# Optimization experiments

Measured on AMD Instinct MI355X. Metric: run time of the kernel, lower is better.

The kernel has to match this reference:

```python
import jax, jax.numpy as jnp
import numpy as np

DIM = 1024
HEADS = 16
HEAD_DIM = DIM // HEADS
MLP_HID = 4 * DIM
EPS = 1e-5


def layer_norm(x, g, b):
    mu = jnp.mean(x, axis=-1, keepdims=True)
    var = jnp.mean(jnp.square(x - mu), axis=-1, keepdims=True)
    return (x - mu) * jax.lax.rsqrt(var + EPS) * g + b


def setup_inputs() -> dict:
    key = jax.random.key(0)
    ks = jax.random.split(key, 8)
    s_in = 1.0 / np.sqrt(DIM)
    s_hid = 1.0 / np.sqrt(MLP_HID)
    return {
        "x": jax.random.normal(ks[0], (4, 2048, DIM), dtype=jnp.float32),
        "qkv_w": jax.random.uniform(ks[1], (3 * DIM, DIM), jnp.float32, -s_in, s_in),
        "proj_w": jax.random.uniform(ks[2], (DIM, DIM), jnp.float32, -s_in, s_in),
        "proj_b": jnp.zeros((DIM,), jnp.float32),
        "ln1_g": jnp.ones((DIM,), jnp.float32),
        "ln1_b": jnp.zeros((DIM,), jnp.float32),
        "w1": jax.random.uniform(ks[3], (MLP_HID, DIM), jnp.float32, -s_in, s_in),
        "b1": jnp.zeros((MLP_HID,), jnp.float32),
        "prelu_a": jnp.asarray(0.25, jnp.float32),
        "w2": jax.random.uniform(ks[4], (DIM, MLP_HID), jnp.float32, -s_hid, s_hid),
        "b2": jnp.zeros((DIM,), jnp.float32),
        "ln2_g": jnp.ones((DIM,), jnp.float32),
        "ln2_b": jnp.zeros((DIM,), jnp.float32),
    }


def reference(x, qkv_w, proj_w, proj_b, ln1_g, ln1_b, w1, b1, prelu_a, w2, b2, ln2_g, ln2_b):
    B, N, C = x.shape
    scale = HEAD_DIM ** (-0.5)

    # Multi-head self-attention (full NxN scores, softmax over keys)
    qkv = (x @ qkv_w.T).reshape(B, N, 3, HEADS, HEAD_DIM)
    qkv = jnp.transpose(qkv, (2, 0, 3, 1, 4))  # [3, B, H, N, hd]
    q, k, v = qkv[0] * scale, qkv[1], qkv[2]
    attn = jax.nn.softmax(jnp.einsum("bhnd,bhmd->bhnm", q, k), axis=-1)
    o = jnp.einsum("bhnm,bhmd->bhnd", attn, v)
    o = jnp.transpose(o, (0, 2, 1, 3)).reshape(B, N, C)
    o = o @ proj_w.T + proj_b

    # Post-norm residual 1
    x = layer_norm(x + o, ln1_g, ln1_b)

    # MLP: Linear -> (Dropout=identity in eval) -> PReLU -> Linear
    h = x @ w1.T + b1
    h = jnp.where(h >= 0, h, prelu_a * h)
    h = h @ w2.T + b2

    # Post-norm residual 2
    return layer_norm(x + h, ln2_g, ln2_b)
```

## Files before the change

### kernel.cpp

```cpp
#include <hip/hip_runtime.h>


typedef __attribute__((ext_vector_type(8))) short short8;
typedef __attribute__((ext_vector_type(4))) short short4v;
typedef __attribute__((ext_vector_type(4))) float floatx4;
typedef __attribute__((ext_vector_type(4))) int int4v;

__device__ __forceinline__ float bf2f(unsigned short u) {
    return __uint_as_float(((unsigned int)u) << 16);
}
__device__ __forceinline__ unsigned short f2bf(float f) {
    unsigned int u = __float_as_uint(f);
    u += 0x7FFFu + ((u >> 16) & 1u);
    return (unsigned short)(u >> 16);
}
__device__ __forceinline__ int pack2bf(float a, float b) {
    return (int)f2bf(a) | ((int)f2bf(b) << 16);
}
__device__ __forceinline__ unsigned int cvt_pk_bf16(float lo, float hi) {
    unsigned int r;
    asm("v_cvt_pk_bf16_f32 %0, %1, %2" : "=v"(r) : "v"(lo), "v"(hi));
    return r;
}

#define Q_PRESCALE 0.18033688011112043f

#if __has_builtin(__builtin_amdgcn_exp2f)
__device__ __forceinline__ float fast_exp2(float x) { return __builtin_amdgcn_exp2f(x); }
#else
__device__ __forceinline__ float fast_exp2(float x) { return __expf(x * 0.6931471805599453f); }
#endif

#if __has_builtin(__builtin_amdgcn_permlane32_swap) && __has_builtin(__builtin_amdgcn_permlane16_swap)
#define HAVE_PERMLANE 1
#else
#define HAVE_PERMLANE 0
#endif

__device__ __forceinline__ void async16(const unsigned short* g, unsigned short* l) {
    __builtin_amdgcn_global_load_lds(
        (const __attribute__((address_space(1))) unsigned int*)g,
        (__attribute__((address_space(3))) unsigned int*)l, 16, 0, 0);
}

#define BARRIER() do { __builtin_amdgcn_s_barrier(); asm volatile("" ::: "memory"); } while (0)
#define VMCNT(n)  asm volatile("s_waitcnt vmcnt(" #n ")" ::: "memory")
#define LGKM0()   asm volatile("s_waitcnt lgkmcnt(0)" ::: "memory")

__global__ __launch_bounds__(256)
void cvt_all(const float* __restrict__ x, const float* __restrict__ qkv_w,
             const float* __restrict__ proj_w, const float* __restrict__ w1,
             const float* __restrict__ w2,
             unsigned short* __restrict__ xb, unsigned short* __restrict__ wb) {
    const int b = blockIdx.x;
    const float* src;
    unsigned short* dst;
    size_t doff;
    if (b < 8192) {
        src = x + (size_t)b * 1024; dst = xb; doff = (size_t)b * 1024;
    } else {
        const int wk = b - 8192;
        dst = wb; doff = (size_t)wk * 1024;
        if (wk < 3072)      src = qkv_w  + (size_t)wk * 1024;
        else if (wk < 4096) src = proj_w + (size_t)(wk - 3072) * 1024;
        else if (wk < 8192) src = w1     + (size_t)(wk - 4096) * 1024;
        else                src = w2     + (size_t)(wk - 8192) * 1024;
    }
    const int t4 = threadIdx.x * 4;
    float4 v = *(const float4*)&src[t4];
    short4v o;
    o[0] = (short)f2bf(v.x); o[1] = (short)f2bf(v.y);
    o[2] = (short)f2bf(v.z); o[3] = (short)f2bf(v.w);
    *(short4v*)&dst[doff + t4] = o;
}

__global__ __launch_bounds__(512, 2)
void gemm128(const unsigned short* __restrict__ A,
             const unsigned short* __restrict__ W,
             const float* __restrict__ bias,
             const float* __restrict__ prelu,
             unsigned short* __restrict__ C,
             int N, int K, int qcols, int NNT) {
    __shared__ alignas(16) unsigned short lA[2][128 * 64];
    __shared__ alignas(16) unsigned short lB[2][256 * 64];

    const int nwg = gridDim.x;
    const int orig = blockIdx.x;
    const int q8 = nwg >> 3, r8 = nwg & 7, xx = orig & 7, rest = orig >> 3;
    const int wgid = (xx < r8 ? xx * (q8 + 1) : r8 * (q8 + 1) + (xx - r8) * q8) + rest;
    const int mt = wgid / NNT, nt = wgid % NNT;
    const int m0 = mt * 128, n0 = nt * 256;

    const int tid  = threadIdx.x;
    const int lane = tid & 63;
    const int wave = tid >> 6;
    const int lr = lane & 15, lq = lane >> 4;
    const int wrow = (wave >> 2) * 64;
    const int wcol = (wave & 3) * 32;
    const int srow = lane >> 3;
    const int scol = ((lane & 7) ^ srow) << 3;
    const int kx = lr & 7;

    const int NT = K >> 6;

    floatx4 acc[2][4][2] = {};
    short8 af[4][2], b0[2][2], b1[2][2];

    auto stA = [&](int d, int tt) {
        #pragma unroll
        for (int it = 0; it < 2; ++it) {
            const int rb = (wave * 2 + it) * 8;
            async16(&A[(size_t)(m0 + rb + srow) * K + tt * 64 + scol], &lA[d][rb * 64]);
        }
    };
    auto stB = [&](int d, int tt, int h) {
        #pragma unroll
        for (int it = 0; it < 2; ++it) {
            const int rb = (wave * 2 + it) * 8;
            async16(&W[(size_t)(n0 + h * 128 + rb + srow) * K + tt * 64 + scol],
                    &lB[d][(h * 128 + rb) * 64]);
        }
    };

#define RD_AF(dd)                                                              \
    _Pragma("unroll") for (int i = 0; i < 4; ++i)                              \
    _Pragma("unroll") for (int s = 0; s < 2; ++s)                              \
        af[i][s] = *(const short8*)&lA[dd][(wrow + i * 16 + lr) * 64 +         \
                                           (((s * 4 + lq) ^ kx) << 3)]
#define RD_B0(dd)                                                              \
    _Pragma("unroll") for (int j = 0; j < 2; ++j)                              \
    _Pragma("unroll") for (int s = 0; s < 2; ++s)                              \
        b0[j][s] = *(const short8*)&lB[dd][(wcol + j * 16 + lr) * 64 +         \
                                           (((s * 4 + lq) ^ kx) << 3)]
#define RD_B1(dd)                                                              \
    _Pragma("unroll") for (int j = 0; j < 2; ++j)                              \
    _Pragma("unroll") for (int s = 0; s < 2; ++s)                              \
        b1[j][s] = *(const short8*)&lB[dd][(128 + wcol + j * 16 + lr) * 64 +   \
                                           (((s * 4 + lq) ^ kx) << 3)]
#define MM128(nh, BB)                                                          \
    _Pragma("unroll") for (int s = 0; s < 2; ++s)                              \
    _Pragma("unroll") for (int i = 0; i < 4; ++i)                              \
    _Pragma("unroll") for (int j = 0; j < 2; ++j)                              \
        acc[nh][i][j] = __builtin_amdgcn_mfma_f32_16x16x32_bf16(               \
            af[i][s], BB[j][s], acc[nh][i][j], 0, 0, 0)

    stA(0, 0); stB(0, 0, 0); stB(0, 0, 1);
    stA(1, 1); stB(1, 1, 0);
    VMCNT(4);
    BARRIER();

    auto tile = [&](int t, int d, int e) {
        RD_AF(d);
        RD_B0(d);
        if (t + 1 < NT) stB(e, t + 1, 1);
        BARRIER();
        LGKM0();
        __builtin_amdgcn_s_setprio(1);
        MM128(0, b0);
        __builtin_amdgcn_s_setprio(0);
        BARRIER();

        RD_B1(d);
        if (t + 2 < NT) { stA(d, t + 2); stB(d, t + 2, 0); }
        BARRIER();
        LGKM0();
        __builtin_amdgcn_s_setprio(1);
        MM128(1, b1);
        __builtin_amdgcn_s_setprio(0);
        if (t + 2 < NT)      { VMCNT(4); }
        else if (t + 1 < NT) { VMCNT(0); }
        BARRIER();
    };

    for (int t = 0; t < NT; t += 2) {
        tile(t, 0, 1);
        tile(t + 1, 1, 0);
    }

#undef RD_AF
#undef RD_B0
#undef RD_B1
#undef MM128

    const bool hasb = (bias != nullptr);
    const bool hasp = (prelu != nullptr);
    const float slope = hasp ? prelu[0] : 0.f;
    #pragma unroll
    for (int nh = 0; nh < 2; ++nh)
        #pragma unroll
        for (int j = 0; j < 2; ++j) {
            const int gc = n0 + nh * 128 + wcol + j * 16 + lr;
            const float bv = hasb ? bias[gc] : 0.f;
            const float cs = (gc < qcols) ? Q_PRESCALE : 1.f;
            #pragma unroll
            for (int i = 0; i < 4; ++i) {
                const int gr = m0 + wrow + i * 16 + lq * 4;
                #pragma unroll
                for (int r = 0; r < 4; ++r) {
                    float v = acc[nh][i][j][r] + bv;
                    if (hasp && v < 0.f) v *= slope;
                    C[(size_t)(gr + r) * N + gc] = f2bf(v * cs);
                }
            }
        }
}

__global__ __launch_bounds__(256, 2)
void gemm_sq(const unsigned short* __restrict__ A,
             const unsigned short* __restrict__ W,
             const float* __restrict__ bias,
             const float* __restrict__ prelu,
             unsigned short* __restrict__ C,
             int N, int K, int qcols, int NNT) {
    __shared__ alignas(16) unsigned short lA[2][128 * 64];
    __shared__ alignas(16) unsigned short lB[2][128 * 64];

    const int nwg = gridDim.x;
    const int orig = blockIdx.x;
    const int q8 = nwg >> 3, r8 = nwg & 7, xx = orig & 7, rest = orig >> 3;
    const int wgid = (xx < r8 ? xx * (q8 + 1) : r8 * (q8 + 1) + (xx - r8) * q8) + rest;
    const int mt = wgid / NNT, nt = wgid % NNT;
    const int m0 = mt * 128, n0 = nt * 128;

    const int tid  = threadIdx.x;
    const int lane = tid & 63;
    const int wave = tid >> 6;
    const int lr = lane & 15, lq = lane >> 4;
    const int wrow = (wave >> 1) * 64;
    const int wcol = (wave & 1) * 64;
    const int srow = lane >> 3;
    const int scol = ((lane & 7) ^ srow) << 3;
    const int kx = lr & 7;

    const int NT = K >> 6;

    floatx4 acc[4][4] = {};
    short8 af[4][2], b0[2][2], b1[2][2];

    auto stA = [&](int d, int tt) {
        #pragma unroll
        for (int it = 0; it < 4; ++it) {
            const int rb = it * 32 + wave * 8;
            async16(&A[(size_t)(m0 + rb + srow) * K + tt * 64 + scol], &lA[d][rb * 64]);
        }
    };
    auto stB = [&](int d, int tt) {
        #pragma unroll
        for (int it = 0; it < 4; ++it) {
            const int rb = it * 32 + wave * 8;
            async16(&W[(size_t)(n0 + rb + srow) * K + tt * 64 + scol], &lB[d][rb * 64]);
        }
    };

#define RD_AF(dd)                                                              \
    _Pragma("unroll") for (int i = 0; i < 4; ++i)                              \
    _Pragma("unroll") for (int s = 0; s < 2; ++s)                              \
        af[i][s] = *(const short8*)&lA[dd][(wrow + i * 16 + lr) * 64 +         \
                                           (((s * 4 + lq) ^ kx) << 3)]
#define RD_B0(dd)                                                              \
    _Pragma("unroll") for (int j = 0; j < 2; ++j)                              \
    _Pragma("unroll") for (int s = 0; s < 2; ++s)                              \
        b0[j][s] = *(const short8*)&lB[dd][(wcol + j * 16 + lr) * 64 +         \
                                           (((s * 4 + lq) ^ kx) << 3)]
#define RD_B1(dd)                                                              \
    _Pragma("unroll") for (int j = 0; j < 2; ++j)                              \
    _Pragma("unroll") for (int s = 0; s < 2; ++s)                              \
        b1[j][s] = *(const short8*)&lB[dd][(wcol + 32 + j * 16 + lr) * 64 +    \
                                           (((s * 4 + lq) ^ kx) << 3)]
#define MMSQ(jb, BB)                                                           \
    _Pragma("unroll") for (int s = 0; s < 2; ++s)                              \
    _Pragma("unroll") for (int i = 0; i < 4; ++i)                              \
    _Pragma("unroll") for (int j = 0; j < 2; ++j)                              \
        acc[i][(jb) + j] = __builtin_amdgcn_mfma_f32_16x16x32_bf16(            \
            af[i][s], BB[j][s], acc[i][(jb) + j], 0, 0, 0)

    stA(0, 0); stB(0, 0);
    VMCNT(0);
    BARRIER();

    auto tile = [&](int t, int d, int e) {
        RD_AF(d);
        RD_B0(d);
        if (t + 1 < NT) stA(e, t + 1);
        BARRIER();
        LGKM0();
        __builtin_amdgcn_s_setprio(1);
        MMSQ(0, b0);
        __builtin_amdgcn_s_setprio(0);
        BARRIER();

        RD_B1(d);
        if (t + 1 < NT) stB(e, t + 1);
        BARRIER();
        LGKM0();
        __builtin_amdgcn_s_setprio(1);
        MMSQ(2, b1);
        __builtin_amdgcn_s_setprio(0);
        VMCNT(0);
        BARRIER();
    };

    for (int t = 0; t < NT; t += 2) {
        tile(t, 0, 1);
        tile(t + 1, 1, 0);
    }

#undef RD_AF
#undef RD_B0
#undef RD_B1
#undef MMSQ

    const bool hasb = (bias != nullptr);
    const bool hasp = (prelu != nullptr);
    const float slope = hasp ? prelu[0] : 0.f;
    #pragma unroll
    for (int j = 0; j < 4; ++j) {
        const int gc = n0 + wcol + j * 16 + lr;
        const float bv = hasb ? bias[gc] : 0.f;
        const float cs = (gc < qcols) ? Q_PRESCALE : 1.f;
        #pragma unroll
        for (int i = 0; i < 4; ++i) {
            const int gr = m0 + wrow + i * 16 + lq * 4;
            #pragma unroll
            for (int r = 0; r < 4; ++r) {
                float v = acc[i][j][r] + bv;
                if (hasp && v < 0.f) v *= slope;
                C[(size_t)(gr + r) * N + gc] = f2bf(v * cs);
            }
        }
    }
}

__global__ __launch_bounds__(256)
void transpose_v(const unsigned short* __restrict__ qkv,
                 unsigned short* __restrict__ vt) {
    const int kt = blockIdx.x;
    const int bh = blockIdx.y;
    const int b = bh >> 4, h = bh & 15;
    __shared__ unsigned short tile[64 * 65];
    for (int t = threadIdx.x; t < 512; t += 256) {
        const int key = t >> 3, c8 = (t & 7) << 3;
        short8 v8 = *(const short8*)&qkv[((size_t)(b * 2048 + kt * 64 + key)) * 3072 +
                                         2048 + h * 64 + c8];
        #pragma unroll
        for (int e = 0; e < 8; ++e)
            tile[key * 65 + c8 + e] = (unsigned short)v8[e];
    }
    __syncthreads();
    for (int t = threadIdx.x; t < 512; t += 256) {
        const int d = t >> 3, k8 = (t & 7) << 3;
        short8 o;
        #pragma unroll
        for (int e = 0; e < 8; ++e)
            o[e] = (short)tile[(k8 + e) * 65 + d];
        *(short8*)&vt[((size_t)bh * 64 + d) * 2048 + kt * 64 + k8] = o;
    }
}

__global__ __launch_bounds__(256, 2)
void attn_kernel(const unsigned short* __restrict__ qkv,
                 const unsigned short* __restrict__ vt,
                 unsigned short* __restrict__ o_attn) {
    const int id = blockIdx.x;
    const int qg = id >> 6;
    const int bh = id & 63;
    const int b = bh >> 4, h = bh & 15;
    const int tid  = threadIdx.x;
    const int lane = tid & 63;
    const int wave = tid >> 6;
    const int lr = lane & 15;
    const int lq = lane >> 4;
    const int q0 = (qg * 4 + wave) * 64;
    const size_t row0 = (size_t)(b * 2048) * 3072;

    __shared__ alignas(16) unsigned short lK[2][64 * 64];
    __shared__ alignas(16) unsigned short lV[2][64 * 64];

    short8 qf[4][2];
    #pragma unroll
    for (int j = 0; j < 4; ++j)
        #pragma unroll
        for (int s = 0; s < 2; ++s)
            qf[j][s] = *(const short8*)&qkv[row0 + (size_t)(q0 + j * 16 + lr) * 3072 +
                                            h * 64 + s * 32 + lq * 8];

    floatx4 oacc[4][4] = {};
    float l_i[4] = {0.f, 0.f, 0.f, 0.f};

    const int srow = lane >> 3;
    const int scol = (((lane & 7) ^ srow)) << 3;
    const int kx = lr & 7;

    auto stage = [&](int bi, int kc) {
        #pragma unroll
        for (int it2 = 0; it2 < 2; ++it2) {
            const int it = wave * 2 + it2;
            const int row = it * 8 + srow;
            async16(&qkv[row0 + (size_t)(kc + row) * 3072 + 1024 + h * 64 + scol],
                    &lK[bi][it * 512 + lane * 8]);
            async16(&vt[((size_t)bh * 64 + row) * 2048 + kc + scol],
                    &lV[bi][it * 512 + lane * 8]);
        }
    };

    asm volatile("s_waitcnt vmcnt(0)" ::: "memory");
    stage(0, 0);

    #pragma unroll 1
    for (int c = 0; c < 32; ++c) {
        const int cur = c & 1;
        if (c + 1 < 32) {
            stage(cur ^ 1, (c + 1) * 64);
            asm volatile("s_waitcnt vmcnt(4)" ::: "memory");
        } else {
            asm volatile("s_waitcnt vmcnt(0)" ::: "memory");
        }
        __builtin_amdgcn_s_barrier();
        asm volatile("" ::: "memory");

        floatx4 sacc[4][4] = {};
        #pragma unroll
        for (int s = 0; s < 2; ++s) {
            short8 kf[4];
            #pragma unroll
            for (int i = 0; i < 4; ++i) {
                const int r = i * 16 + lr;
                kf[i] = *(const short8*)&lK[cur][r * 64 + (((s * 4 + lq) ^ kx) << 3)];
            }
            __builtin_amdgcn_s_setprio(1);
            #pragma unroll
            for (int i = 0; i < 4; ++i)
                #pragma unroll
                for (int j = 0; j < 4; ++j)
                    sacc[i][j] = __builtin_amdgcn_mfma_f32_16x16x32_bf16(
                        kf[i], qf[j][s], sacc[i][j], 0, 0, 0);
            __builtin_amdgcn_s_setprio(0);
        }

        unsigned int pkd[4][4][2];
        #pragma unroll
        for (int i = 0; i < 4; ++i)
            #pragma unroll
            for (int j = 0; j < 4; ++j) {
                const float e0 = fast_exp2(sacc[i][j][0]);
                const float e1 = fast_exp2(sacc[i][j][1]);
                const float e2 = fast_exp2(sacc[i][j][2]);
                const float e3 = fast_exp2(sacc[i][j][3]);
                l_i[j] += (e0 + e1) + (e2 + e3);
                pkd[i][j][0] = cvt_pk_bf16(e0, e1);
                pkd[i][j][1] = cvt_pk_bf16(e2, e3);
            }

        #pragma unroll
        for (int s = 0; s < 2; ++s) {
            short8 vf[4];
            #pragma unroll
            for (int i = 0; i < 4; ++i) {
                const int r = i * 16 + lr;
                vf[i] = *(const short8*)&lV[cur][r * 64 + (((s * 4 + lq) ^ kx) << 3)];
            }
            short8 bq[4];
            #pragma unroll
            for (int j = 0; j < 4; ++j) {
                int4v iv;
#if HAVE_PERMLANE
                auto p0 = __builtin_amdgcn_permlane32_swap(
                    pkd[2 * s][j][0], pkd[2 * s + 1][j][0], false, false);
                auto w0 = __builtin_amdgcn_permlane16_swap(p0[0], p0[1], false, false);
                auto p1 = __builtin_amdgcn_permlane32_swap(
                    pkd[2 * s][j][1], pkd[2 * s + 1][j][1], false, false);
                auto w1 = __builtin_amdgcn_permlane16_swap(p1[0], p1[1], false, false);
                iv[0] = (int)w0[0]; iv[1] = (int)w1[0];
                iv[2] = (int)w0[1]; iv[3] = (int)w1[1];
#else
                const int src0 = lr + ((lq & 1) * 2) * 16;
                const int src1 = src0 + 16;
                const bool hi = (lq >> 1) != 0;
                int a0 = __shfl((int)pkd[2 * s][j][0], src0, 64);
                int c0 = __shfl((int)pkd[2 * s + 1][j][0], src0, 64);
                int a1 = __shfl((int)pkd[2 * s][j][1], src0, 64);
                int c1 = __shfl((int)pkd[2 * s + 1][j][1], src0, 64);
                int a2 = __shfl((int)pkd[2 * s][j][0], src1, 64);
                int c2 = __shfl((int)pkd[2 * s + 1][j][0], src1, 64);
                int a3 = __shfl((int)pkd[2 * s][j][1], src1, 64);
                int c3 = __shfl((int)pkd[2 * s + 1][j][1], src1, 64);
                iv[0] = hi ? c0 : a0;
                iv[1] = hi ? c1 : a1;
                iv[2] = hi ? c2 : a2;
                iv[3] = hi ? c3 : a3;
#endif
                bq[j] = __builtin_bit_cast(short8, iv);
            }
            __builtin_amdgcn_s_setprio(1);
            #pragma unroll
            for (int j = 0; j < 4; ++j)
                #pragma unroll
                for (int i = 0; i < 4; ++i)
                    oacc[i][j] = __builtin_amdgcn_mfma_f32_16x16x32_bf16(
                        vf[i], bq[j], oacc[i][j], 0, 0, 0);
            __builtin_amdgcn_s_setprio(0);
        }

        asm volatile("s_waitcnt lgkmcnt(0)" ::: "memory");
        __builtin_amdgcn_s_barrier();
        asm volatile("" ::: "memory");
    }

    #pragma unroll
    for (int j = 0; j < 4; ++j) {
        l_i[j] += __shfl_xor(l_i[j], 16, 64);
        l_i[j] += __shfl_xor(l_i[j], 32, 64);
        const float rl = 1.f / l_i[j];
        const int q = q0 + j * 16 + lr;
        #pragma unroll
        for (int i = 0; i < 4; ++i) {
            int2 pk;
            pk.x = pack2bf(oacc[i][j][0] * rl, oacc[i][j][1] * rl);
            pk.y = pack2bf(oacc[i][j][2] * rl, oacc[i][j][3] * rl);
            *(int2*)&o_attn[((size_t)(b * 2048 + q)) * 1024 + h * 64 + i * 16 + lq * 4] = pk;
        }
    }
}

__global__ __launch_bounds__(256)
void ln_f32_bf16(const float* __restrict__ x,
                 const unsigned short* __restrict__ res,
                 const float* __restrict__ g,
                 const float* __restrict__ bta,
                 unsigned short* __restrict__ out) {
    const int row = blockIdx.x;
    const int t = threadIdx.x;
    const size_t base = (size_t)row * 1024;

    float4 xv = *(const float4*)&x[base + t * 4];
    short4v rv = *(const short4v*)&res[base + t * 4];
    float v[4] = { xv.x + bf2f((unsigned short)rv[0]),
                   xv.y + bf2f((unsigned short)rv[1]),
                   xv.z + bf2f((unsigned short)rv[2]),
                   xv.w + bf2f((unsigned short)rv[3]) };
    float s = 0.f, s2 = 0.f;
    #pragma unroll
    for (int k = 0; k < 4; ++k) { s += v[k]; s2 += v[k] * v[k]; }
    #pragma unroll
    for (int off = 32; off > 0; off >>= 1) {
        s  += __shfl_xor(s, off, 64);
        s2 += __shfl_xor(s2, off, 64);
    }
    __shared__ float red[8];
    const int wave = t >> 6;
    if ((t & 63) == 0) { red[wave] = s; red[4 + wave] = s2; }
    __syncthreads();
    s  = red[0] + red[1] + red[2] + red[3];
    s2 = red[4] + red[5] + red[6] + red[7];
    const float mean = s * (1.f / 1024.f);
    const float var  = fmaxf(s2 * (1.f / 1024.f) - mean * mean, 0.f);
    const float inv  = rsqrtf(var + 1e-5f);

    short4v ov;
    #pragma unroll
    for (int k = 0; k < 4; ++k) {
        int c = t * 4 + k;
        ov[k] = (short)f2bf((v[k] - mean) * inv * g[c] + bta[c]);
    }
    *(short4v*)&out[base + t * 4] = ov;
}

__global__ __launch_bounds__(256)
void ln_bf16_f32(const unsigned short* __restrict__ x,
                 const unsigned short* __restrict__ res,
                 const float* __restrict__ g,
                 const float* __restrict__ bta,
                 float* __restrict__ out) {
    const int row = blockIdx.x;
    const int t = threadIdx.x;
    const size_t base = (size_t)row * 1024;

    short4v xv = *(const short4v*)&x[base + t * 4];
    short4v rv = *(const short4v*)&res[base + t * 4];
    float v[4];
    float s = 0.f, s2 = 0.f;
    #pragma unroll
    for (int k = 0; k < 4; ++k) {
        v[k] = bf2f((unsigned short)xv[k]) + bf2f((unsigned short)rv[k]);
        s += v[k];
        s2 += v[k] * v[k];
    }
    #pragma unroll
    for (int off = 32; off > 0; off >>= 1) {
        s  += __shfl_xor(s, off, 64);
        s2 += __shfl_xor(s2, off, 64);
    }
    __shared__ float red[8];
    const int wave = t >> 6;
    if ((t & 63) == 0) { red[wave] = s; red[4 + wave] = s2; }
    __syncthreads();
    s  = red[0] + red[1] + red[2] + red[3];
    s2 = red[4] + red[5] + red[6] + red[7];
    const float mean = s * (1.f / 1024.f);
    const float var  = fmaxf(s2 * (1.f / 1024.f) - mean * mean, 0.f);
    const float inv  = rsqrtf(var + 1e-5f);

    float4 ov;
    ov.x = (v[0] - mean) * inv * g[t * 4 + 0] + bta[t * 4 + 0];
    ov.y = (v[1] - mean) * inv * g[t * 4 + 1] + bta[t * 4 + 1];
    ov.z = (v[2] - mean) * inv * g[t * 4 + 2] + bta[t * 4 + 2];
    ov.w = (v[3] - mean) * inv * g[t * 4 + 3] + bta[t * 4 + 3];
    *(float4*)&out[base + t * 4] = ov;
}

extern "C" void kernel_launch(void* const* d_in, const int* in_sizes, int n_in,
                              void* d_out, int out_size, void* d_ws, size_t ws_size,
                              hipStream_t stream) {
    const float* x      = (const float*)d_in[0];
    const float* qkv_w  = (const float*)d_in[1];
    const float* proj_w = (const float*)d_in[2];
    const float* proj_b = (const float*)d_in[3];
    const float* ln1_g  = (const float*)d_in[4];
    const float* ln1_b  = (const float*)d_in[5];
    const float* w1     = (const float*)d_in[6];
    const float* b1     = (const float*)d_in[7];
    const float* prelu  = (const float*)d_in[8];
    const float* w2     = (const float*)d_in[9];
    const float* b2     = (const float*)d_in[10];
    const float* ln2_g  = (const float*)d_in[11];
    const float* ln2_b  = (const float*)d_in[12];
    float* out = (float*)d_out;

    char* ws = (char*)d_ws;
    const size_t MB = 1024 * 1024;
    unsigned short* wqkvb  = (unsigned short*)(ws);
    unsigned short* wprojb = (unsigned short*)(ws + 6 * MB);
    unsigned short* w1b    = (unsigned short*)(ws + 8 * MB);
    unsigned short* w2b    = (unsigned short*)(ws + 16 * MB);
    unsigned short* xb     = (unsigned short*)(ws + 24 * MB);
    unsigned short* vtb    = (unsigned short*)(ws + 24 * MB);
    unsigned short* qkvb   = (unsigned short*)(ws + 40 * MB);
    unsigned short* oat    = (unsigned short*)(ws + 88 * MB);
    unsigned short* pout   = (unsigned short*)(ws + 24 * MB);
    unsigned short* x1b    = (unsigned short*)(ws + 40 * MB);
    unsigned short* h1     = (unsigned short*)(ws + 56 * MB);
    unsigned short* h2     = (unsigned short*)(ws + 24 * MB);

    cvt_all<<<20480, 256, 0, stream>>>(x, qkv_w, proj_w, w1, w2,
                                       xb, (unsigned short*)ws);

    gemm128<<<dim3(64 * 12), 512, 0, stream>>>(xb, wqkvb, nullptr, nullptr,
                                               qkvb, 3072, 1024, 1024, 12);
    transpose_v<<<dim3(32, 64), 256, 0, stream>>>(qkvb, vtb);
    attn_kernel<<<512, 256, 0, stream>>>(qkvb, vtb, oat);
    gemm_sq<<<dim3(64 * 8), 256, 0, stream>>>(oat, wprojb, proj_b, nullptr,
                                              pout, 1024, 1024, 0, 8);
    ln_f32_bf16<<<8192, 256, 0, stream>>>(x, pout, ln1_g, ln1_b, x1b);
    gemm128<<<dim3(64 * 16), 512, 0, stream>>>(x1b, w1b, b1, prelu,
                                               h1, 4096, 1024, 0, 16);
    gemm_sq<<<dim3(64 * 8), 256, 0, stream>>>(h1, w2b, b2, nullptr,
                                              h2, 1024, 4096, 0, 8);
    ln_bf16_f32<<<8192, 256, 0, stream>>>(x1b, h2, ln2_g, ln2_b, out);
}
```

Measured before the change: 493.3 us.

## Enlarge MLP up-projection GEMM tile to 256x256 and route QKV GEMM to gemm_sq

Turns the 128x256 GEMM kernel into a 256x256 tile with four quarter-step MFMA phases per K-tile, interleaving async loads and LDS reads for the next tile so A and B fragments are reused across both halves. The W1 GEMM uses this larger tile, halving its workgroup count and increasing arithmetic intensity per byte loaded. The QKV projection switches to the square 128x128 gemm_sq kernel with 24 column tiles. LDS use doubles to 128KB per block and accumulator registers double, which may reduce occupancy or cause spills, and fewer workgroups can leave compute units underused.

```diff
diff --git a/kernel.cpp b/kernel.cpp
--- a/kernel.cpp
+++ b/kernel.cpp
@@ -75,13 +75,13 @@
 }
 
 __global__ __launch_bounds__(512, 2)
-void gemm128(const unsigned short* __restrict__ A,
+void gemm256(const unsigned short* __restrict__ A,
              const unsigned short* __restrict__ W,
              const float* __restrict__ bias,
              const float* __restrict__ prelu,
              unsigned short* __restrict__ C,
              int N, int K, int qcols, int NNT) {
-    __shared__ alignas(16) unsigned short lA[2][128 * 64];
+    __shared__ alignas(16) unsigned short lA[2][256 * 64];
     __shared__ alignas(16) unsigned short lB[2][256 * 64];
 
     const int nwg = gridDim.x;
@@ -89,7 +89,7 @@
     const int q8 = nwg >> 3, r8 = nwg & 7, xx = orig & 7, rest = orig >> 3;
     const int wgid = (xx < r8 ? xx * (q8 + 1) : r8 * (q8 + 1) + (xx - r8) * q8) + rest;
     const int mt = wgid / NNT, nt = wgid % NNT;
-    const int m0 = mt * 128, n0 = nt * 256;
+    const int m0 = mt * 256, n0 = nt * 256;
 
     const int tid  = threadIdx.x;
     const int lane = tid & 63;
@@ -103,29 +103,28 @@
 
     const int NT = K >> 6;
 
-    floatx4 acc[2][4][2] = {};
+    floatx4 acc[2][2][4][2] = {};
     short8 af[4][2], b0[2][2], b1[2][2];
 
-    auto stA = [&](int d, int tt) {
+    auto stA = [&](int d, int tt, int h) {
         #pragma unroll
         for (int it = 0; it < 2; ++it) {
-            const int rb = (wave * 2 + it) * 8;
+            const int rb = h * 128 + (wave * 2 + it) * 8;
             async16(&A[(size_t)(m0 + rb + srow) * K + tt * 64 + scol], &lA[d][rb * 64]);
         }
     };
     auto stB = [&](int d, int tt, int h) {
         #pragma unroll
         for (int it = 0; it < 2; ++it) {
-            const int rb = (wave * 2 + it) * 8;
-            async16(&W[(size_t)(n0 + h * 128 + rb + srow) * K + tt * 64 + scol],
-                    &lB[d][(h * 128 + rb) * 64]);
+            const int rb = h * 128 + (wave * 2 + it) * 8;
+            async16(&W[(size_t)(n0 + rb + srow) * K + tt * 64 + scol], &lB[d][rb * 64]);
         }
     };
 
-#define RD_AF(dd)                                                              \
+#define RD_AF(dd, half)                                                        \
     _Pragma("unroll") for (int i = 0; i < 4; ++i)                              \
     _Pragma("unroll") for (int s = 0; s < 2; ++s)                              \
-        af[i][s] = *(const short8*)&lA[dd][(wrow + i * 16 + lr) * 64 +         \
+        af[i][s] = *(const short8*)&lA[dd][((half) * 128 + wrow + i * 16 + lr) * 64 + \
                                            (((s * 4 + lq) ^ kx) << 3)]
 #define RD_B0(dd)                                                              \
     _Pragma("unroll") for (int j = 0; j < 2; ++j)                              \
@@ -137,39 +136,56 @@
     _Pragma("unroll") for (int s = 0; s < 2; ++s)                              \
         b1[j][s] = *(const short8*)&lB[dd][(128 + wcol + j * 16 + lr) * 64 +   \
                                            (((s * 4 + lq) ^ kx) << 3)]
-#define MM128(nh, BB)                                                          \
+#define MM256(mh, nh, BB)                                                      \
     _Pragma("unroll") for (int s = 0; s < 2; ++s)                              \
     _Pragma("unroll") for (int i = 0; i < 4; ++i)                              \
     _Pragma("unroll") for (int j = 0; j < 2; ++j)                              \
-        acc[nh][i][j] = __builtin_amdgcn_mfma_f32_16x16x32_bf16(               \
-            af[i][s], BB[j][s], acc[nh][i][j], 0, 0, 0)
-
-    stA(0, 0); stB(0, 0, 0); stB(0, 0, 1);
-    stA(1, 1); stB(1, 1, 0);
-    VMCNT(4);
+        acc[mh][nh][i][j] = __builtin_amdgcn_mfma_f32_16x16x32_bf16(           \
+            af[i][s], BB[j][s], acc[mh][nh][i][j], 0, 0, 0)
+
+    stA(0, 0, 0); stB(0, 0, 0); stB(0, 0, 1); stA(0, 0, 1);
+    stA(1, 1, 0); stB(1, 1, 0); stB(1, 1, 1);
+    VMCNT(6);
     BARRIER();
+    RD_AF(0, 0);
+    RD_B0(0);
 
     auto tile = [&](int t, int d, int e) {
-        RD_AF(d);
-        RD_B0(d);
-        if (t + 1 < NT) stB(e, t + 1, 1);
-        BARRIER();
-        LGKM0();
+        RD_B1(d);
+        if (t + 1 < NT) stA(e, t + 1, 1);
+        BARRIER();
         __builtin_amdgcn_s_setprio(1);
-        MM128(0, b0);
+        MM256(0, 0, b0);
         __builtin_amdgcn_s_setprio(0);
         BARRIER();
 
-        RD_B1(d);
-        if (t + 2 < NT) { stA(d, t + 2); stB(d, t + 2, 0); }
-        BARRIER();
-        LGKM0();
+        if (t + 2 < NT) stA(d, t + 2, 0);
+        BARRIER();
         __builtin_amdgcn_s_setprio(1);
-        MM128(1, b1);
+        MM256(0, 1, b1);
+        __builtin_amdgcn_s_setprio(0);
+        RD_AF(d, 1);
+        BARRIER();
+
+        if (t + 2 < NT) stB(d, t + 2, 0);
+        BARRIER();
+        __builtin_amdgcn_s_setprio(1);
+        MM256(1, 1, b1);
         __builtin_amdgcn_s_setprio(0);
         if (t + 2 < NT)      { VMCNT(4); }
         else if (t + 1 < NT) { VMCNT(0); }
         BARRIER();
+
+        if (t + 2 < NT) stB(d, t + 2, 1);
+        BARRIER();
+        __builtin_amdgcn_s_setprio(1);
+        MM256(1, 0, b0);
+        __builtin_amdgcn_s_setprio(0);
+        if (t + 1 < NT) {
+            RD_AF(e, 0);
+            RD_B0(e);
+        }
+        BARRIER();
     };
 
     for (int t = 0; t < NT; t += 2) {
@@ -180,29 +196,31 @@
 #undef RD_AF
 #undef RD_B0
 #undef RD_B1
-#undef MM128
+#undef MM256
 
     const bool hasb = (bias != nullptr);
     const bool hasp = (prelu != nullptr);
     const float slope = hasp ? prelu[0] : 0.f;
     #pragma unroll
-    for (int nh = 0; nh < 2; ++nh)
-        #pragma unroll
-        for (int j = 0; j < 2; ++j) {
-            const int gc = n0 + nh * 128 + wcol + j * 16 + lr;
-            const float bv = hasb ? bias[gc] : 0.f;
-            const float cs = (gc < qcols) ? Q_PRESCALE : 1.f;
-            #pragma unroll
-            for (int i = 0; i < 4; ++i) {
-                const int gr = m0 + wrow + i * 16 + lq * 4;
+    for (int mh = 0; mh < 2; ++mh)
+        #pragma unroll
+        for (int nh = 0; nh < 2; ++nh)
+            #pragma unroll
+            for (int j = 0; j < 2; ++j) {
+                const int gc = n0 + nh * 128 + wcol + j * 16 + lr;
+                const float bv = hasb ? bias[gc] : 0.f;
+                const float cs = (gc < qcols) ? Q_PRESCALE : 1.f;
                 #pragma unroll
-                for (int r = 0; r < 4; ++r) {
-                    float v = acc[nh][i][j][r] + bv;
-                    if (hasp && v < 0.f) v *= slope;
-                    C[(size_t)(gr + r) * N + gc] = f2bf(v * cs);
+                for (int i = 0; i < 4; ++i) {
+                    const int gr = m0 + mh * 128 + wrow + i * 16 + lq * 4;
+                    #pragma unroll
+                    for (int r = 0; r < 4; ++r) {
+                        float v = acc[mh][nh][i][j][r] + bv;
+                        if (hasp && v < 0.f) v *= slope;
+                        C[(size_t)(gr + r) * N + gc] = f2bf(v * cs);
+                    }
                 }
             }
-        }
 }
 
 __global__ __launch_bounds__(256, 2)
@@ -644,14 +662,14 @@
     cvt_all<<<20480, 256, 0, stream>>>(x, qkv_w, proj_w, w1, w2,
                                        xb, (unsigned short*)ws);
 
-    gemm128<<<dim3(64 * 12), 512, 0, stream>>>(xb, wqkvb, nullptr, nullptr,
-                                               qkvb, 3072, 1024, 1024, 12);
+    gemm_sq<<<dim3(64 * 24), 256, 0, stream>>>(xb, wqkvb, nullptr, nullptr,
+                                               qkvb, 3072, 1024, 1024, 24);
     transpose_v<<<dim3(32, 64), 256, 0, stream>>>(qkvb, vtb);
     attn_kernel<<<512, 256, 0, stream>>>(qkvb, vtb, oat);
     gemm_sq<<<dim3(64 * 8), 256, 0, stream>>>(oat, wprojb, proj_b, nullptr,
                                               pout, 1024, 1024, 0, 8);
     ln_f32_bf16<<<8192, 256, 0, stream>>>(x, pout, ln1_g, ln1_b, x1b);
-    gemm128<<<dim3(64 * 16), 512, 0, stream>>>(x1b, w1b, b1, prelu,
+    gemm256<<<dim3(32 * 16), 512, 0, stream>>>(x1b, w1b, b1, prelu,
                                                h1, 4096, 1024, 0, 16);
     gemm_sq<<<dim3(64 * 8), 256, 0, stream>>>(h1, w2b, b2, nullptr,
                                               h2, 1024, 4096, 0, 8);
```

After: 472.6 us. 1.04x faster.
